# Optimization experiments

Measured on AMD Instinct MI355X. Metric: run time of the kernel, lower is better.

## Reference

```python
import jax, jax.numpy as jnp
import numpy as np
from jax import lax

B, C, H, W = 8, 256, 64, 64
O, K, E = 256, 3, 3  # out_channels, kernel_size, num_experts

def setup_inputs() -> dict:
    key = jax.random.key(0)
    k1, k2, k3, k4, k5 = jax.random.split(key, 5)
    q = jax.random.normal(k1, (B, C, H, W), dtype=jnp.float32)
    y = jax.random.normal(k2, (B, C, H, W), dtype=jnp.float32)
    experts = jax.random.normal(k3, (E, O, 2 * C, K, K), dtype=jnp.float32)
    # torch nn.Linear(2C, E): store transposed [2C, E] for ctx @ gate_w
    bound = 1.0 / np.sqrt(2 * C)
    gate_w = jax.random.uniform(k4, (2 * C, E), minval=-bound, maxval=bound, dtype=jnp.float32)
    gate_b = jax.random.uniform(k5, (E,), minval=-bound, maxval=bound, dtype=jnp.float32)
    return {"q": q, "y": y, "experts": experts, "gate_w": gate_w, "gate_b": gate_b}

def reference(q, y, experts, gate_w, gate_b):
    # gate: softmax over experts from global-avg-pooled context of y (duplicated)
    y_ctx = jnp.mean(y, axis=(2, 3))                       # [B, C]
    context = jnp.concatenate([y_ctx, y_ctx], axis=1)       # [B, 2C]
    gates = jax.nn.softmax(context @ gate_w + gate_b, axis=1)  # [B, E]
    # per-sample fused kernel: sum_e gates[b,e] * experts[e]  -> [B, O, 2C, K, K]
    w = jnp.einsum('be,eoikl->boikl', gates, experts)
    xy = jnp.concatenate([q, q], axis=1)                     # [B, 2C, H, W]
    # batched dynamic conv via grouped conv: batch -> groups (no Python loop)
    b, c2, h, wd = xy.shape
    x1 = xy.reshape(1, b * c2, h, wd)
    w1 = w.reshape(b * O, c2, K, K)
    out = lax.conv_general_dilated(
        x1, w1, window_strides=(1, 1), padding='SAME',
        dimension_numbers=('NCHW', 'OIHW', 'NCHW'),
        feature_group_count=b)
    return out.reshape(b, O, h, wd)
```

## Files before the change

kernel.cpp:

```cpp
#include <hip/hip_runtime.h>
#include <hip/hip_bf16.h>
#include <math.h>


typedef __bf16 bf16x8 __attribute__((ext_vector_type(8)));
typedef __bf16 bf16x4 __attribute__((ext_vector_type(4)));
typedef float f32x4 __attribute__((ext_vector_type(4)));

#define AS1 __attribute__((address_space(1)))
#define AS3 __attribute__((address_space(3)))

__global__ __launch_bounds__(64) void yctx_kernel(const float* __restrict__ y,
                                                  float* __restrict__ yctx) {
  int bc = blockIdx.x;
  const float4* p = (const float4*)(y + (size_t)bc * 4096);
  int lane = threadIdx.x;
  float s = 0.f;
  for (int i = lane; i < 1024; i += 64) {
    float4 v = p[i];
    s += v.x + v.y + v.z + v.w;
  }
#pragma unroll
  for (int off = 32; off > 0; off >>= 1) s += __shfl_down(s, off, 64);
  if (lane == 0) yctx[bc] = s * (1.f / 4096.f);
}

__global__ __launch_bounds__(64) void logits_kernel(const float* __restrict__ yctx,
                                                    const float* __restrict__ gw,
                                                    const float* __restrict__ gb,
                                                    float* __restrict__ logits) {
  int be = blockIdx.x;
  int b = be / 3, e = be - b * 3;
  int lane = threadIdx.x;
  float s = 0.f;
  for (int c = lane; c < 256; c += 64)
    s += yctx[b * 256 + c] * (gw[c * 3 + e] + gw[(c + 256) * 3 + e]);
#pragma unroll
  for (int off = 32; off > 0; off >>= 1) s += __shfl_down(s, off, 64);
  if (lane == 0) logits[be] = s + gb[e];
}

__global__ __launch_bounds__(256) void wbuild_kernel(const float* __restrict__ experts,
                                                     const float* __restrict__ logits,
                                                     __bf16* __restrict__ wf) {
  int o = blockIdx.x;
  int tid = threadIdx.x;
  __shared__ float sf[3][2304];
  __shared__ float g[8][3];

#pragma unroll
  for (int e = 0; e < 3; e++) {
    const float4* src = (const float4*)(experts + ((size_t)e * 256 + o) * 4608);
    float4* dstp = (float4*)sf[e];
    for (int i = tid; i < 576; i += 256) {
      float4 a = src[i], bq = src[i + 576];
      float4 r;
      r.x = a.x + bq.x; r.y = a.y + bq.y; r.z = a.z + bq.z; r.w = a.w + bq.w;
      dstp[i] = r;
    }
  }
  if (tid < 8) {
    float l0 = logits[tid * 3 + 0], l1 = logits[tid * 3 + 1], l2 = logits[tid * 3 + 2];
    float m = fmaxf(l0, fmaxf(l1, l2));
    float e0 = __expf(l0 - m), e1 = __expf(l1 - m), e2 = __expf(l2 - m);
    float inv = 1.f / (e0 + e1 + e2);
    g[tid][0] = e0 * inv; g[tid][1] = e1 * inv; g[tid][2] = e2 * inv;
  }
  __syncthreads();

  int cl = tid & 31, ch = tid >> 5;
#pragma unroll 1
  for (int b = 0; b < 8; b++) {
    float g0 = g[b][0], g1 = g[b][1], g2 = g[b][2];
#pragma unroll
    for (int tap = 0; tap < 9; tap++) {
      float v = g0 * sf[0][tid * 9 + tap] + g1 * sf[1][tid * 9 + tap] +
                g2 * sf[2][tid * 9 + tap];
      wf[((((size_t)b * 9 + tap) * 8 + ch) * 256 + o) * 32 + cl] = (__bf16)v;
    }
  }
}

__global__ __launch_bounds__(256) void qt_kernel(const float* __restrict__ q,
                                                 __bf16* __restrict__ qT) {
  int bid = blockIdx.x;
  int hp = bid % 66;
  int t2 = bid / 66;
  int ch = t2 & 7;
  int b = t2 >> 3;
  __bf16* dst = qT + (((size_t)(b * 8 + ch) * 66 + hp) * 66) * 32;
  int tid = threadIdx.x;
  float4 z4 = {0.f, 0.f, 0.f, 0.f};
  if (hp == 0 || hp == 65) {
    float4* d4 = (float4*)dst;
    for (int i = tid; i < 264; i += 256) d4[i] = z4;
    return;
  }
  __shared__ float tile2[64][33];
  int h = hp - 1;
  {
    int w = tid & 63, ci = tid >> 6;
#pragma unroll
    for (int j = 0; j < 8; j++) {
      int c = ci * 8 + j;
      tile2[w][c] = q[(((size_t)b * 256 + ch * 32 + c) * 64 + h) * 64 + w];
    }
  }
  if (tid < 4) ((float4*)dst)[tid] = z4;
  else if (tid < 8) ((float4*)(dst + 65 * 32))[tid - 4] = z4;
  __syncthreads();

  int a = tid & 7, wsl = tid >> 3;
  int cl4 = a * 4;
#pragma unroll
  for (int k = 0; k < 2; k++) {
    int w = wsl * 2 + k, wp = w + 1;
    int clp4 = (((cl4 >> 3) ^ ((wp >> 1) & 3)) << 3) | (cl4 & 7);
    float v0 = tile2[w][cl4 + 0], v1 = tile2[w][cl4 + 1];
    float v2 = tile2[w][cl4 + 2], v3 = tile2[w][cl4 + 3];
    bf16x4 r = {(__bf16)v0, (__bf16)v1, (__bf16)v2, (__bf16)v3};
    *(bf16x4*)(dst + wp * 32 + clp4) = r;
  }
}

__global__ __launch_bounds__(256) void conv_kernel(const __bf16* __restrict__ qT,
                                                   const __bf16* __restrict__ wf,
                                                   float* __restrict__ out) {
  __shared__ __align__(16) __bf16 Qlds[2][4 * 66 * 32];
  const int tid = threadIdx.x;
  const int lane = tid & 63;
  const int wv = tid >> 6;
  const int wm = wv >> 1, wn = wv & 1;
  const int l15 = lane & 15, qd = lane >> 4;

  const int bid = blockIdx.x;
  const int b = bid & 7;
  const int rem = bid >> 3;
  const int o0 = (rem >> 5) * 128;
  const int h0 = (rem & 31) * 2;

  f32x4 acc[4][4];
  {
    f32x4 z = {0.f, 0.f, 0.f, 0.f};
#pragma unroll
    for (int i = 0; i < 4; i++)
#pragma unroll
      for (int j = 0; j < 4; j++) acc[i][j] = z;
  }

  const char* qT_b = (const char*)qT + (size_t)b * 8 * 66 * 66 * 32 * 2;
  const char* abase = (const char*)wf + ((size_t)b * 9 * 8 * 256 +
                                         (size_t)(o0 + wm * 64 + l15)) * 64 +
                      (size_t)qd * 16;
  bf16x8 acur[4], anxt[4];

  {
    const char* qsrc = qT_b + ((size_t)h0) * 66 * 32 * 2;
    for (int i = tid; i < 1056; i += 256) {
      int ub = i - lane;
      __builtin_amdgcn_global_load_lds((const AS1 void*)(qsrc + ((size_t)i << 4)),
                                       (AS3 void*)((char*)Qlds[0] + ((size_t)ub << 4)),
                                       16, 0, 0);
    }
#pragma unroll
    for (int mi = 0; mi < 4; mi++)
      acur[mi] = *(const bf16x8*)(abase + mi * 1024);
    __syncthreads();
  }

#pragma unroll 1
  for (int ch = 0; ch < 8; ch++) {
    if (ch < 7) {
      const char* qsrc = qT_b + ((size_t)(ch + 1) * 66 + h0) * 66 * 32 * 2;
      char* qdst = (char*)Qlds[(ch + 1) & 1];
      for (int i = tid; i < 1056; i += 256) {
        int ub = i - lane;
        __builtin_amdgcn_global_load_lds((const AS1 void*)(qsrc + ((size_t)i << 4)),
                                         (AS3 void*)(qdst + ((size_t)ub << 4)),
                                         16, 0, 0);
      }
    }
    const char* Qb = (const char*)Qlds[ch & 1];
#pragma unroll
    for (int tap = 0; tap < 9; tap++) {
      {
        int tapn = (tap == 8) ? 0 : tap + 1;
        int chn = (tap == 8) ? ch + 1 : ch;
        size_t aoff = ((size_t)(tapn * 8 + chn)) << 14;
#pragma unroll
        for (int mi = 0; mi < 4; mi++)
          anxt[mi] = *(const bf16x8*)(abase + aoff + mi * 1024);
      }
      const int dh = tap / 3, dw = tap - dh * 3;
      const int r = wn + dh;
#pragma unroll
      for (int ni = 0; ni < 4; ni++) {
        int wp = ni * 16 + l15 + dw;
        int g = (qd ^ ((wp >> 1) & 3)) << 3;
        bf16x8 bfv = *(const bf16x8*)(Qb + ((r * 66 + wp) * 32 + g) * 2);
#pragma unroll
        for (int mi = 0; mi < 4; mi++)
          acc[mi][ni] = __builtin_amdgcn_mfma_f32_16x16x32_bf16(
              acur[mi], bfv, acc[mi][ni], 0, 0, 0);
      }
#pragma unroll
      for (int mi = 0; mi < 4; mi++) acur[mi] = anxt[mi];
    }
    __syncthreads();
  }

  const int hh = h0 + wn;
#pragma unroll
  for (int mi = 0; mi < 4; mi++) {
    int o = o0 + wm * 64 + mi * 16 + qd * 4;
#pragma unroll
    for (int ni = 0; ni < 4; ni++) {
      int w = ni * 16 + l15;
#pragma unroll
      for (int rr = 0; rr < 4; rr++)
        out[(((size_t)b * 256 + (o + rr)) * 64 + hh) * 64 + w] = acc[mi][ni][rr];
    }
  }
}

extern "C" void kernel_launch(void* const* d_in, const int* in_sizes, int n_in,
                              void* d_out, int out_size, void* d_ws, size_t ws_size,
                              hipStream_t stream) {
  (void)in_sizes; (void)n_in; (void)out_size; (void)ws_size;
  const float* q = (const float*)d_in[0];
  const float* y = (const float*)d_in[1];
  const float* experts = (const float*)d_in[2];
  const float* gate_w = (const float*)d_in[3];
  const float* gate_b = (const float*)d_in[4];
  float* out = (float*)d_out;

  char* ws = (char*)d_ws;
  float* yctx = (float*)ws;
  float* logits = (float*)(ws + 8192);
  __bf16* wf = (__bf16*)(ws + 16384);
  __bf16* qT = (__bf16*)(ws + 16384 + 9437184);

  yctx_kernel<<<2048, 64, 0, stream>>>(y, yctx);
  logits_kernel<<<24, 64, 0, stream>>>(yctx, gate_w, gate_b, logits);
  qt_kernel<<<8 * 8 * 66, 256, 0, stream>>>(q, qT);
  wbuild_kernel<<<256, 256, 0, stream>>>(experts, logits, wf);
  conv_kernel<<<512, 256, 0, stream>>>(qT, wf, out);
}
```

Measured before the change: 179.7 us.

## Fuse gate logits into wbuild and deepen conv weight prefetch pipeline

Removes the separate logits kernel by computing the gating logits redundantly inside each wbuild block, saving one launch. In the conv kernel, weight fragments are now prefetched two taps ahead using a three-slot register ring instead of one tap ahead. The next channel's input tile load is split across the first two taps instead of being issued all at once. The deeper ring raises register pressure, and the 256 wbuild blocks now each repeat the small gate dot product.

```diff
diff --git a/kernel.cpp b/kernel.cpp
--- a/kernel.cpp
+++ b/kernel.cpp
@@ -25,28 +25,38 @@
   if (lane == 0) yctx[bc] = s * (1.f / 4096.f);
 }
 
-__global__ __launch_bounds__(64) void logits_kernel(const float* __restrict__ yctx,
-                                                    const float* __restrict__ gw,
-                                                    const float* __restrict__ gb,
-                                                    float* __restrict__ logits) {
-  int be = blockIdx.x;
-  int b = be / 3, e = be - b * 3;
-  int lane = threadIdx.x;
-  float s = 0.f;
-  for (int c = lane; c < 256; c += 64)
-    s += yctx[b * 256 + c] * (gw[c * 3 + e] + gw[(c + 256) * 3 + e]);
-#pragma unroll
-  for (int off = 32; off > 0; off >>= 1) s += __shfl_down(s, off, 64);
-  if (lane == 0) logits[be] = s + gb[e];
-}
-
 __global__ __launch_bounds__(256) void wbuild_kernel(const float* __restrict__ experts,
-                                                     const float* __restrict__ logits,
+                                                     const float* __restrict__ yctx,
+                                                     const float* __restrict__ gw,
+                                                     const float* __restrict__ gb,
                                                      __bf16* __restrict__ wf) {
   int o = blockIdx.x;
   int tid = threadIdx.x;
   __shared__ float sf[3][2304];
+  __shared__ float lg[8][3];
   __shared__ float g[8][3];
+
+  {
+    int lb = tid >> 5, li = tid & 31;
+    float p0 = 0.f, p1 = 0.f, p2 = 0.f;
+#pragma unroll
+    for (int j = 0; j < 8; j++) {
+      int c = li + j * 32;
+      float yv = yctx[lb * 256 + c];
+      p0 += yv * (gw[c * 3 + 0] + gw[(c + 256) * 3 + 0]);
+      p1 += yv * (gw[c * 3 + 1] + gw[(c + 256) * 3 + 1]);
+      p2 += yv * (gw[c * 3 + 2] + gw[(c + 256) * 3 + 2]);
+    }
+#pragma unroll
+    for (int off = 16; off > 0; off >>= 1) {
+      p0 += __shfl_down(p0, off, 32);
+      p1 += __shfl_down(p1, off, 32);
+      p2 += __shfl_down(p2, off, 32);
+    }
+    if (li == 0) {
+      lg[lb][0] = p0 + gb[0]; lg[lb][1] = p1 + gb[1]; lg[lb][2] = p2 + gb[2];
+    }
+  }
 
 #pragma unroll
   for (int e = 0; e < 3; e++) {
@@ -59,8 +69,9 @@
       dstp[i] = r;
     }
   }
+  __syncthreads();
   if (tid < 8) {
-    float l0 = logits[tid * 3 + 0], l1 = logits[tid * 3 + 1], l2 = logits[tid * 3 + 2];
+    float l0 = lg[tid][0], l1 = lg[tid][1], l2 = lg[tid][2];
     float m = fmaxf(l0, fmaxf(l1, l2));
     float e0 = __expf(l0 - m), e1 = __expf(l1 - m), e2 = __expf(l2 - m);
     float inv = 1.f / (e0 + e1 + e2);
@@ -152,7 +163,7 @@
   const char* abase = (const char*)wf + ((size_t)b * 9 * 8 * 256 +
                                          (size_t)(o0 + wm * 64 + l15)) * 64 +
                       (size_t)qd * 16;
-  bf16x8 acur[4], anxt[4];
+  bf16x8 areg[3][4];
 
   {
     const char* qsrc = qT_b + ((size_t)h0) * 66 * 32 * 2;
@@ -163,33 +174,44 @@
                                        16, 0, 0);
     }
 #pragma unroll
-    for (int mi = 0; mi < 4; mi++)
-      acur[mi] = *(const bf16x8*)(abase + mi * 1024);
+    for (int mi = 0; mi < 4; mi++) {
+      areg[0][mi] = *(const bf16x8*)(abase + mi * 1024);
+      areg[1][mi] = *(const bf16x8*)(abase + ((size_t)8 << 14) + mi * 1024);
+    }
     __syncthreads();
   }
 
 #pragma unroll 1
   for (int ch = 0; ch < 8; ch++) {
-    if (ch < 7) {
-      const char* qsrc = qT_b + ((size_t)(ch + 1) * 66 + h0) * 66 * 32 * 2;
-      char* qdst = (char*)Qlds[(ch + 1) & 1];
-      for (int i = tid; i < 1056; i += 256) {
-        int ub = i - lane;
-        __builtin_amdgcn_global_load_lds((const AS1 void*)(qsrc + ((size_t)i << 4)),
-                                         (AS3 void*)(qdst + ((size_t)ub << 4)),
-                                         16, 0, 0);
-      }
-    }
     const char* Qb = (const char*)Qlds[ch & 1];
+    const char* qsrc_n = qT_b + ((size_t)(ch + 1) * 66 + h0) * 66 * 32 * 2;
+    char* qdst_n = (char*)Qlds[(ch + 1) & 1];
 #pragma unroll
     for (int tap = 0; tap < 9; tap++) {
       {
-        int tapn = (tap == 8) ? 0 : tap + 1;
-        int chn = (tap == 8) ? ch + 1 : ch;
+        int tapn = (tap + 2 >= 9) ? tap - 7 : tap + 2;
+        int chn = (tap + 2 >= 9) ? ch + 1 : ch;
         size_t aoff = ((size_t)(tapn * 8 + chn)) << 14;
 #pragma unroll
         for (int mi = 0; mi < 4; mi++)
-          anxt[mi] = *(const bf16x8*)(abase + aoff + mi * 1024);
+          areg[(tap + 2) % 3][mi] = *(const bf16x8*)(abase + aoff + mi * 1024);
+      }
+      if (ch < 7) {
+        if (tap == 0) {
+          for (int i = tid; i < 512; i += 256) {
+            int ub = i - lane;
+            __builtin_amdgcn_global_load_lds((const AS1 void*)(qsrc_n + ((size_t)i << 4)),
+                                             (AS3 void*)(qdst_n + ((size_t)ub << 4)),
+                                             16, 0, 0);
+          }
+        } else if (tap == 1) {
+          for (int i = 512 + tid; i < 1056; i += 256) {
+            int ub = i - lane;
+            __builtin_amdgcn_global_load_lds((const AS1 void*)(qsrc_n + ((size_t)i << 4)),
+                                             (AS3 void*)(qdst_n + ((size_t)ub << 4)),
+                                             16, 0, 0);
+          }
+        }
       }
       const int dh = tap / 3, dw = tap - dh * 3;
       const int r = wn + dh;
@@ -201,10 +223,8 @@
 #pragma unroll
         for (int mi = 0; mi < 4; mi++)
           acc[mi][ni] = __builtin_amdgcn_mfma_f32_16x16x32_bf16(
-              acur[mi], bfv, acc[mi][ni], 0, 0, 0);
+              areg[tap % 3][mi], bfv, acc[mi][ni], 0, 0, 0);
       }
-#pragma unroll
-      for (int mi = 0; mi < 4; mi++) acur[mi] = anxt[mi];
     }
     __syncthreads();
   }
@@ -236,13 +256,11 @@
 
   char* ws = (char*)d_ws;
   float* yctx = (float*)ws;
-  float* logits = (float*)(ws + 8192);
   __bf16* wf = (__bf16*)(ws + 16384);
   __bf16* qT = (__bf16*)(ws + 16384 + 9437184);
 
   yctx_kernel<<<2048, 64, 0, stream>>>(y, yctx);
-  logits_kernel<<<24, 64, 0, stream>>>(yctx, gate_w, gate_b, logits);
   qt_kernel<<<8 * 8 * 66, 256, 0, stream>>>(q, qT);
-  wbuild_kernel<<<256, 256, 0, stream>>>(experts, logits, wf);
+  wbuild_kernel<<<256, 256, 0, stream>>>(experts, yctx, gate_w, gate_b, wf);
   conv_kernel<<<512, 256, 0, stream>>>(qT, wf, out);
 }
```

Result: no change. 178.7 us (-0.5%).
